# Performance work log

Hardware: AMD Instinct MI355X
Metric: run time of the kernel (lower is better)

Reference implementation:

```python
import jax, jax.numpy as jnp
import numpy as np

N = 100000       # nodes
E = 3200000      # edges (before self-loops)
F_IN = 256       # input feature dim
HID = 32         # GCNConv output dim
CLASSES = 10


def setup_inputs() -> dict:
    key = jax.random.key(0)
    k1, k2, k3, k4 = jax.random.split(key, 4)
    feature = jax.random.normal(k1, (N, F_IN), dtype=jnp.float32)
    edge_index = jax.random.randint(k2, (2, E), 0, N, dtype=jnp.int64)
    W1 = jax.random.normal(k3, (F_IN, HID), dtype=jnp.float32) * (1.0 / np.sqrt(F_IN))
    b1 = jnp.zeros((HID,), dtype=jnp.float32)
    W2 = jax.random.normal(k4, (HID, CLASSES), dtype=jnp.float32) * (1.0 / np.sqrt(HID))
    b2 = jnp.zeros((CLASSES,), dtype=jnp.float32)
    return {"feature": feature, "edge_index": edge_index,
            "W1": W1, "b1": b1, "W2": W2, "b2": b2}


def reference(feature, edge_index, W1, b1, W2, b2):
    # --- GCNConv(features, 32): PyG semantics ---
    # add self-loops
    loops = jnp.arange(N, dtype=edge_index.dtype)
    row = jnp.concatenate([edge_index[0], loops])   # source nodes
    col = jnp.concatenate([edge_index[1], loops])   # target nodes
    # linear transform before propagation
    h = feature @ W1                                # [N, HID]
    # symmetric deg^{-1/2} normalization (degree counted at targets)
    deg = jax.ops.segment_sum(jnp.ones_like(col, dtype=h.dtype), col,
                              num_segments=N)       # [N], >=1 due to self-loops
    dinv = jax.lax.rsqrt(deg)
    norm = dinv[row] * dinv[col]                    # [E+N]
    # gather-scale-scatter aggregation
    msg = h[row] * norm[:, None]                    # [E+N, HID]
    agg = jax.ops.segment_sum(msg, col, num_segments=N) + b1  # [N, HID]
    # --- relu, (dropout: identity in eval), final linear, log_softmax ---
    act = jax.nn.relu(agg)
    logits = act @ W2 + b2                          # [N, CLASSES]
    return jax.nn.log_softmax(logits, axis=1)
```

## Files before the change

kernel.cpp:

```cpp
#include <hip/hip_runtime.h>

constexpr int N_NODES = 100000;
constexpr int E_EDGES = 3200000;
constexpr int F_IN    = 256;
constexpr int HID     = 32;
constexpr int NCLS    = 10;

constexpr int BUCK_SHIFT = 7;
constexpr int NPB        = 128;
constexpr int NBUCK      = (N_NODES + NPB - 1) / NPB;
constexpr int EPB        = 8192;
constexpr int NBLK1      = (E_EDGES + EPB - 1) / EPB;
constexpr int CAP        = 6144;

constexpr size_t OFF_FLAG = 0;
constexpr size_t OFF_GCUR = 4u << 10;
constexpr size_t OFF_BB   = 8u << 10;
constexpr size_t OFF_W1F  = 32u << 10;
constexpr size_t OFF_CNT  = 4u << 20;
constexpr size_t OFF_OFF  = 5u << 20;
constexpr size_t OFF_DINV = 6u << 20;
constexpr size_t OFF_CSR  = 7u << 20;
constexpr size_t OFF_BIN  = 20u << 20;
constexpr size_t OFF_HS   = 20u << 20;

typedef __attribute__((ext_vector_type(8))) short bf16x8;
typedef __attribute__((ext_vector_type(4))) float f32x4;

__device__ __forceinline__ unsigned pack_bf16x2(float a, float b) {
    unsigned ua = __float_as_uint(a), ub = __float_as_uint(b);
    ua = (ua + 0x7FFFu + ((ua >> 16) & 1u)) >> 16;
    ub = (ub + 0x7FFFu + ((ub >> 16) & 1u)) >> 16;
    return ua | (ub << 16);
}
__device__ __forceinline__ unsigned short bf16_rne(float x) {
    unsigned u = __float_as_uint(x);
    return (unsigned short)((u + 0x7FFFu + ((u >> 16) & 1u)) >> 16);
}
__device__ __forceinline__ float bf16_lo(unsigned p) { return __uint_as_float(p << 16); }
__device__ __forceinline__ float bf16_hi(unsigned p) { return __uint_as_float(p & 0xFFFF0000u); }

__device__ __forceinline__ int load_idx(const void* ei, long long i, int is64) {
    if (is64) return (int)((const long long*)ei)[i];
    return ((const int*)ei)[i];
}

__global__ __launch_bounds__(1024) void k_init(const int* __restrict__ ei32,
                                               int* __restrict__ flag,
                                               int* __restrict__ gcur) {
    __shared__ int nz;
    int tid = threadIdx.x;
    if (tid == 0) nz = 0;
    __syncthreads();
    if (ei32[2 * tid + 1] != 0) atomicOr(&nz, 1);
    __syncthreads();
    if (tid == 0) flag[0] = (nz == 0) ? 1 : 0;
    if (tid < NBUCK) gcur[tid] = tid * CAP;
}

__global__ void k_w1frag(const float* __restrict__ W1, unsigned* __restrict__ w1f) {
    int tid = threadIdx.x;
    for (int i = tid; i < 16 * 64 * 4; i += 256) {
        int p    = i & 3;
        int lane = (i >> 2) & 63;
        int f    = i >> 8;
        int ks = f >> 1, t = f & 1;
        int kg = lane >> 4, col = lane & 15;
        int k0 = ks * 32 + kg * 8 + p * 2;
        float w0 = W1[k0 * HID + t * 16 + col];
        float w1 = W1[(k0 + 1) * HID + t * 16 + col];
        w1f[i] = pack_bf16x2(w0, w1);
    }
}

__global__ __launch_bounds__(1024) void k_scat(const void* __restrict__ ei,
                                               const int* __restrict__ flag,
                                               int* __restrict__ gcur,
                                               unsigned* __restrict__ binned) {
    __shared__ unsigned       sval[EPB];
    __shared__ unsigned short sbuck[EPB];
    __shared__ int h[NBUCK];
    __shared__ int cur[NBUCK];
    int tid = threadIdx.x, blk = blockIdx.x;
    for (int i = tid; i < NBUCK; i += 1024) h[i] = 0;
    __syncthreads();

    int is64 = flag[0];
    int base = blk * EPB;
    int nedge = min(EPB, E_EDGES - base);
    for (int k = tid; k < nedge; k += 1024) {
        int i = base + k;
        int r = load_idx(ei, i, is64);
        int c = load_idx(ei, (long long)E_EDGES + i, is64);
        int b = c >> BUCK_SHIFT;
        sval[k]  = ((unsigned)r << BUCK_SHIFT) | ((unsigned)c & (NPB - 1));
        sbuck[k] = (unsigned short)b;
        atomicAdd(&h[b], 1);
    }
    __syncthreads();

    for (int j = tid; j < NBUCK; j += 1024) {
        int c = h[j];
        cur[j] = (c > 0) ? atomicAdd(&gcur[j], c) : 0;
    }
    __syncthreads();

    for (int k = tid; k < nedge; k += 1024) {
        int d = atomicAdd(&cur[sbuck[k]], 1);
        binned[d] = sval[k];
    }
}

__global__ __launch_bounds__(1024) void k_bscan(const int* __restrict__ gcur,
                                                int* __restrict__ bucketBase) {
    __shared__ int s[1024];
    int tid = threadIdx.x;
    int v = (tid < NBUCK) ? (gcur[tid] - tid * CAP) : 0;
    s[tid] = v;
    __syncthreads();
    for (int d = 1; d < 1024; d <<= 1) {
        int t = (tid >= d) ? s[tid - d] : 0;
        __syncthreads();
        s[tid] += t;
        __syncthreads();
    }
    if (tid < NBUCK) bucketBase[tid] = s[tid] - v;
    if (tid == 1023) bucketBase[NBUCK] = s[1023];
}

__global__ __launch_bounds__(512) void k_p2(const unsigned* __restrict__ binned,
                                            const int* __restrict__ gcur,
                                            const int* __restrict__ bucketBase,
                                            int* __restrict__ cnt,
                                            int* __restrict__ off,
                                            float* __restrict__ dinv,
                                            int* __restrict__ csr) {
    __shared__ int lcnt[NPB], sc[NPB], lcur[NPB];
    int b = blockIdx.x, tid = threadIdx.x;
    int s = b * CAP, e = gcur[b];
    int db = bucketBase[b];
    if (tid < NPB) lcnt[tid] = 0;
    __syncthreads();
    for (int i = s + tid; i < e; i += 512)
        atomicAdd(&lcnt[binned[i] & (NPB - 1)], 1);
    __syncthreads();
    if (tid < NPB) sc[tid] = lcnt[tid];
    __syncthreads();
    for (int d = 1; d < NPB; d <<= 1) {
        int t = 0;
        if (tid < NPB && tid >= d) t = sc[tid - d];
        __syncthreads();
        if (tid < NPB) sc[tid] += t;
        __syncthreads();
    }
    if (tid < NPB) {
        int o = db + sc[tid] - lcnt[tid];
        lcur[tid] = o;
        int node = b * NPB + tid;
        if (node < N_NODES) {
            off[node]  = o;
            cnt[node]  = lcnt[tid];
            dinv[node] = rsqrtf((float)lcnt[tid] + 1.0f);
        }
    }
    __syncthreads();
    for (int i = s + tid; i < e; i += 512) {
        unsigned p = binned[i];
        int pos = atomicAdd(&lcur[p & (NPB - 1)], 1);
        csr[pos] = (int)(p >> BUCK_SHIFT);
    }
}

__global__ __launch_bounds__(256) void k_h(const float* __restrict__ feat,
                                           const unsigned* __restrict__ w1f,
                                           const float* __restrict__ dinv,
                                           unsigned short* __restrict__ hs16s) {
    int tid  = threadIdx.x;
    int lane = tid & 63;
    long wid = (long)blockIdx.x * 4 + (tid >> 6);
    int n0 = (int)(wid * 16);
    if (n0 >= N_NODES) return;

    bf16x8 bfrag[16];
    const bf16x8* wv = (const bf16x8*)w1f;
    #pragma unroll
    for (int f = 0; f < 16; f++) bfrag[f] = wv[f * 64 + lane];

    int arow = lane & 15;
    int kg   = lane >> 4;
    const float4* fr = (const float4*)(feat + (size_t)(n0 + arow) * F_IN);

    f32x4 acc0 = {0.f, 0.f, 0.f, 0.f};
    f32x4 acc1 = {0.f, 0.f, 0.f, 0.f};

    #pragma unroll
    for (int ks = 0; ks < 8; ks++) {
        float4 fa = fr[ks * 8 + kg * 2 + 0];
        float4 fb = fr[ks * 8 + kg * 2 + 1];
        unsigned au[4];
        au[0] = pack_bf16x2(fa.x, fa.y);
        au[1] = pack_bf16x2(fa.z, fa.w);
        au[2] = pack_bf16x2(fb.x, fb.y);
        au[3] = pack_bf16x2(fb.z, fb.w);
        bf16x8 af = *(bf16x8*)au;
        acc0 = __builtin_amdgcn_mfma_f32_16x16x32_bf16(af, bfrag[ks * 2 + 0], acc0, 0, 0, 0);
        acc1 = __builtin_amdgcn_mfma_f32_16x16x32_bf16(af, bfrag[ks * 2 + 1], acc1, 0, 0, 0);
    }

    int rb = kg * 4;
    #pragma unroll
    for (int r = 0; r < 4; r++) {
        int node = n0 + rb + r;
        float di = dinv[node];
        hs16s[(size_t)node * HID + arow]      = bf16_rne(acc0[r] * di);
        hs16s[(size_t)node * HID + 16 + arow] = bf16_rne(acc1[r] * di);
    }
}

__global__ __launch_bounds__(256) void k_aggout(const int* __restrict__ off,
                                                const int* __restrict__ cnt,
                                                const int* __restrict__ csr,
                                                const unsigned* __restrict__ hs16,
                                                const float* __restrict__ dinv,
                                                const float* __restrict__ b1,
                                                const float* __restrict__ W2,
                                                const float* __restrict__ b2,
                                                float* __restrict__ out) {
    __shared__ float W2s[HID * NCLS];
    __shared__ float b2s[NCLS];
    int tid = threadIdx.x;
    for (int i = tid; i < HID * NCLS; i += 256) W2s[i] = W2[i];
    if (tid < NCLS) b2s[tid] = b2[tid];
    __syncthreads();

    int l2   = tid & 3;
    int g    = tid >> 2;
    int node = blockIdx.x * 64 + g;
    if (node >= N_NODES) return;

    int o = off[node];
    int n = cnt[node];

    const uint4* hsv = (const uint4*)hs16;
    uint4 ps = hsv[(size_t)node * 4 + l2];
    float a0 = bf16_lo(ps.x), a1 = bf16_hi(ps.x);
    float a2 = bf16_lo(ps.y), a3 = bf16_hi(ps.y);
    float a4 = bf16_lo(ps.z), a5 = bf16_hi(ps.z);
    float a6 = bf16_lo(ps.w), a7 = bf16_hi(ps.w);

    #define ADDQ(Q) \
        a0 += bf16_lo(Q.x); a1 += bf16_hi(Q.x); a2 += bf16_lo(Q.y); a3 += bf16_hi(Q.y); \
        a4 += bf16_lo(Q.z); a5 += bf16_hi(Q.z); a6 += bf16_lo(Q.w); a7 += bf16_hi(Q.w);

    int i = 0;
    for (; i + 4 <= n; i += 4) {
        int r0 = csr[o + i + 0];
        int r1 = csr[o + i + 1];
        int r2 = csr[o + i + 2];
        int r3 = csr[o + i + 3];
        uint4 q0 = hsv[(size_t)r0 * 4 + l2];
        uint4 q1 = hsv[(size_t)r1 * 4 + l2];
        uint4 q2 = hsv[(size_t)r2 * 4 + l2];
        uint4 q3 = hsv[(size_t)r3 * 4 + l2];
        ADDQ(q0) ADDQ(q1) ADDQ(q2) ADDQ(q3)
    }
    for (; i < n; i++) {
        uint4 q = hsv[(size_t)csr[o + i] * 4 + l2];
        ADDQ(q)
    }
    #undef ADDQ

    float di = dinv[node];
    float4 b1lo = *(const float4*)(b1 + 8 * l2);
    float4 b1hi = *(const float4*)(b1 + 8 * l2 + 4);
    float act[8];
    act[0] = fmaxf(b1lo.x + a0 * di, 0.f);
    act[1] = fmaxf(b1lo.y + a1 * di, 0.f);
    act[2] = fmaxf(b1lo.z + a2 * di, 0.f);
    act[3] = fmaxf(b1lo.w + a3 * di, 0.f);
    act[4] = fmaxf(b1hi.x + a4 * di, 0.f);
    act[5] = fmaxf(b1hi.y + a5 * di, 0.f);
    act[6] = fmaxf(b1hi.z + a6 * di, 0.f);
    act[7] = fmaxf(b1hi.w + a7 * di, 0.f);

    float p[NCLS];
    #pragma unroll
    for (int c = 0; c < NCLS; c++) {
        float s = 0.f;
        #pragma unroll
        for (int k = 0; k < 8; k++) s = fmaf(act[k], W2s[(8 * l2 + k) * NCLS + c], s);
        p[c] = s;
    }

    #pragma unroll
    for (int d = 1; d < 4; d <<= 1) {
        #pragma unroll
        for (int c = 0; c < NCLS; c++) p[c] += __shfl_xor(p[c], d, 4);
    }

    #pragma unroll
    for (int c = 0; c < NCLS; c++) p[c] += b2s[c];
    float m = p[0];
    #pragma unroll
    for (int c = 1; c < NCLS; c++) m = fmaxf(m, p[c]);
    float se = 0.f;
    #pragma unroll
    for (int c = 0; c < NCLS; c++) se += expf(p[c] - m);
    float lse = m + logf(se);

    #pragma unroll
    for (int q = 0; q < 3; q++) {
        int c = l2 + 4 * q;
        if (c < NCLS) {
            float v = p[0];
            #pragma unroll
            for (int cc = 1; cc < NCLS; cc++) v = (c == cc) ? p[cc] : v;
            out[(size_t)node * NCLS + c] = v - lse;
        }
    }
}

extern "C" void kernel_launch(void* const* d_in, const int* in_sizes, int n_in,
                              void* d_out, int out_size, void* d_ws, size_t ws_size,
                              hipStream_t stream) {
    const float* feat = (const float*)d_in[0];
    const void*  ei   = d_in[1];
    const float* W1   = (const float*)d_in[2];
    const float* b1   = (const float*)d_in[3];
    const float* W2   = (const float*)d_in[4];
    const float* b2   = (const float*)d_in[5];
    float* out = (float*)d_out;

    char* ws = (char*)d_ws;
    int*      flag   = (int*)(ws + OFF_FLAG);
    int*      gcur   = (int*)(ws + OFF_GCUR);
    int*      bbase  = (int*)(ws + OFF_BB);
    unsigned* w1f    = (unsigned*)(ws + OFF_W1F);
    int*      cnt    = (int*)(ws + OFF_CNT);
    int*      off    = (int*)(ws + OFF_OFF);
    float*    dinv   = (float*)(ws + OFF_DINV);
    int*      csr    = (int*)(ws + OFF_CSR);
    unsigned* binned = (unsigned*)(ws + OFF_BIN);
    unsigned* hs16   = (unsigned*)(ws + OFF_HS);

    k_init<<<1, 1024, 0, stream>>>((const int*)ei, flag, gcur);
    k_w1frag<<<1, 256, 0, stream>>>(W1, w1f);
    k_scat<<<NBLK1, 1024, 0, stream>>>(ei, flag, gcur, binned);
    k_bscan<<<1, 1024, 0, stream>>>(gcur, bbase);
    k_p2<<<NBUCK, 512, 0, stream>>>(binned, gcur, bbase, cnt, off, dinv, csr);

    k_h<<<(N_NODES / 16 + 3) / 4, 256, 0, stream>>>(feat, w1f, dinv,
                                                    (unsigned short*)hs16);
    k_aggout<<<(N_NODES + 63) / 64, 256, 0, stream>>>(off, cnt, csr, hs16, dinv,
                                                      b1, W2, b2, out);
}
```

Baseline: 132.9 us.

## Store hidden features as fp16 and accumulate with packed half2 adds

Switches the intermediate scaled hidden features from bf16 to fp16 so the aggregation kernel can sum neighbours with packed half2 adds instead of unpacking to fp32. It also widens the gather unroll from 4 to 8 edges for more memory-level parallelism, and merges the W1 fragment packing kernel into the init kernel to save a launch. Accumulating around 33 neighbours in fp16 adds rounding error and overflow risk compared with fp32 accumulation.

```diff
diff --git a/kernel.cpp b/kernel.cpp
--- a/kernel.cpp
+++ b/kernel.cpp
@@ -1,4 +1,5 @@
 #include <hip/hip_runtime.h>
+#include <hip/hip_fp16.h>
 
 constexpr int N_NODES = 100000;
 constexpr int E_EDGES = 3200000;
@@ -33,21 +34,20 @@
     ub = (ub + 0x7FFFu + ((ub >> 16) & 1u)) >> 16;
     return ua | (ub << 16);
 }
-__device__ __forceinline__ unsigned short bf16_rne(float x) {
-    unsigned u = __float_as_uint(x);
-    return (unsigned short)((u + 0x7FFFu + ((u >> 16) & 1u)) >> 16);
-}
-__device__ __forceinline__ float bf16_lo(unsigned p) { return __uint_as_float(p << 16); }
-__device__ __forceinline__ float bf16_hi(unsigned p) { return __uint_as_float(p & 0xFFFF0000u); }
+__device__ __forceinline__ __half2 u2h(unsigned u) {
+    union { unsigned u; __half2 h; } v; v.u = u; return v.h;
+}
 
 __device__ __forceinline__ int load_idx(const void* ei, long long i, int is64) {
     if (is64) return (int)((const long long*)ei)[i];
     return ((const int*)ei)[i];
 }
 
-__global__ __launch_bounds__(1024) void k_init(const int* __restrict__ ei32,
-                                               int* __restrict__ flag,
-                                               int* __restrict__ gcur) {
+__global__ __launch_bounds__(1024) void k_initw(const int* __restrict__ ei32,
+                                                int* __restrict__ flag,
+                                                int* __restrict__ gcur,
+                                                const float* __restrict__ W1,
+                                                unsigned* __restrict__ w1f) {
     __shared__ int nz;
     int tid = threadIdx.x;
     if (tid == 0) nz = 0;
@@ -56,11 +56,10 @@
     __syncthreads();
     if (tid == 0) flag[0] = (nz == 0) ? 1 : 0;
     if (tid < NBUCK) gcur[tid] = tid * CAP;
-}
-
-__global__ void k_w1frag(const float* __restrict__ W1, unsigned* __restrict__ w1f) {
-    int tid = threadIdx.x;
-    for (int i = tid; i < 16 * 64 * 4; i += 256) {
+
+    #pragma unroll
+    for (int q = 0; q < 4; q++) {
+        int i = tid + q * 1024;
         int p    = i & 3;
         int lane = (i >> 2) & 63;
         int f    = i >> 8;
@@ -212,8 +211,8 @@
     for (int r = 0; r < 4; r++) {
         int node = n0 + rb + r;
         float di = dinv[node];
-        hs16s[(size_t)node * HID + arow]      = bf16_rne(acc0[r] * di);
-        hs16s[(size_t)node * HID + 16 + arow] = bf16_rne(acc1[r] * di);
+        hs16s[(size_t)node * HID + arow]      = __half_as_ushort(__float2half(acc0[r] * di));
+        hs16s[(size_t)node * HID + 16 + arow] = __half_as_ushort(__float2half(acc1[r] * di));
     }
 }
 
@@ -243,45 +242,56 @@
 
     const uint4* hsv = (const uint4*)hs16;
     uint4 ps = hsv[(size_t)node * 4 + l2];
-    float a0 = bf16_lo(ps.x), a1 = bf16_hi(ps.x);
-    float a2 = bf16_lo(ps.y), a3 = bf16_hi(ps.y);
-    float a4 = bf16_lo(ps.z), a5 = bf16_hi(ps.z);
-    float a6 = bf16_lo(ps.w), a7 = bf16_hi(ps.w);
+    __half2 s0 = u2h(ps.x), s1 = u2h(ps.y), s2 = u2h(ps.z), s3 = u2h(ps.w);
 
     #define ADDQ(Q) \
-        a0 += bf16_lo(Q.x); a1 += bf16_hi(Q.x); a2 += bf16_lo(Q.y); a3 += bf16_hi(Q.y); \
-        a4 += bf16_lo(Q.z); a5 += bf16_hi(Q.z); a6 += bf16_lo(Q.w); a7 += bf16_hi(Q.w);
+        s0 = __hadd2(s0, u2h(Q.x)); s1 = __hadd2(s1, u2h(Q.y)); \
+        s2 = __hadd2(s2, u2h(Q.z)); s3 = __hadd2(s3, u2h(Q.w));
 
     int i = 0;
-    for (; i + 4 <= n; i += 4) {
+    for (; i + 8 <= n; i += 8) {
         int r0 = csr[o + i + 0];
         int r1 = csr[o + i + 1];
         int r2 = csr[o + i + 2];
         int r3 = csr[o + i + 3];
+        int r4 = csr[o + i + 4];
+        int r5 = csr[o + i + 5];
+        int r6 = csr[o + i + 6];
+        int r7 = csr[o + i + 7];
         uint4 q0 = hsv[(size_t)r0 * 4 + l2];
         uint4 q1 = hsv[(size_t)r1 * 4 + l2];
         uint4 q2 = hsv[(size_t)r2 * 4 + l2];
         uint4 q3 = hsv[(size_t)r3 * 4 + l2];
+        uint4 q4 = hsv[(size_t)r4 * 4 + l2];
+        uint4 q5 = hsv[(size_t)r5 * 4 + l2];
+        uint4 q6 = hsv[(size_t)r6 * 4 + l2];
+        uint4 q7 = hsv[(size_t)r7 * 4 + l2];
         ADDQ(q0) ADDQ(q1) ADDQ(q2) ADDQ(q3)
+        ADDQ(q4) ADDQ(q5) ADDQ(q6) ADDQ(q7)
     }
     for (; i < n; i++) {
         uint4 q = hsv[(size_t)csr[o + i] * 4 + l2];
         ADDQ(q)
     }
     #undef ADDQ
+
+    float2 f0 = __half22float2(s0);
+    float2 f1 = __half22float2(s1);
+    float2 f2 = __half22float2(s2);
+    float2 f3 = __half22float2(s3);
 
     float di = dinv[node];
     float4 b1lo = *(const float4*)(b1 + 8 * l2);
     float4 b1hi = *(const float4*)(b1 + 8 * l2 + 4);
     float act[8];
-    act[0] = fmaxf(b1lo.x + a0 * di, 0.f);
-    act[1] = fmaxf(b1lo.y + a1 * di, 0.f);
-    act[2] = fmaxf(b1lo.z + a2 * di, 0.f);
-    act[3] = fmaxf(b1lo.w + a3 * di, 0.f);
-    act[4] = fmaxf(b1hi.x + a4 * di, 0.f);
-    act[5] = fmaxf(b1hi.y + a5 * di, 0.f);
-    act[6] = fmaxf(b1hi.z + a6 * di, 0.f);
-    act[7] = fmaxf(b1hi.w + a7 * di, 0.f);
+    act[0] = fmaxf(b1lo.x + f0.x * di, 0.f);
+    act[1] = fmaxf(b1lo.y + f0.y * di, 0.f);
+    act[2] = fmaxf(b1lo.z + f1.x * di, 0.f);
+    act[3] = fmaxf(b1lo.w + f1.y * di, 0.f);
+    act[4] = fmaxf(b1hi.x + f2.x * di, 0.f);
+    act[5] = fmaxf(b1hi.y + f2.y * di, 0.f);
+    act[6] = fmaxf(b1hi.z + f3.x * di, 0.f);
+    act[7] = fmaxf(b1hi.w + f3.y * di, 0.f);
 
     float p[NCLS];
     #pragma unroll
@@ -343,8 +353,7 @@
     unsigned* binned = (unsigned*)(ws + OFF_BIN);
     unsigned* hs16   = (unsigned*)(ws + OFF_HS);
 
-    k_init<<<1, 1024, 0, stream>>>((const int*)ei, flag, gcur);
-    k_w1frag<<<1, 256, 0, stream>>>(W1, w1f);
+    k_initw<<<1, 1024, 0, stream>>>((const int*)ei, flag, gcur, W1, w1f);
     k_scat<<<NBLK1, 1024, 0, stream>>>(ei, flag, gcur, binned);
     k_bscan<<<1, 1024, 0, stream>>>(gcur, bbase);
     k_p2<<<NBUCK, 512, 0, stream>>>(binned, gcur, bbase, cnt, off, dinv, csr);
```

New measurement: 122.8 us. 1.08x faster.
